# Performance work log

Measured on AMD Instinct MI355X. Metric: run time of the kernel, lower is better.

The kernel has to match this reference:

```python
import jax, jax.numpy as jnp
import numpy as np

B, N, E, R, D, L = 2, 40000, 400000, 64, 64, 6
LN_EPS = 1e-5


def _layer_norm(x, g, b):
    mu = jnp.mean(x, axis=-1, keepdims=True)
    var = jnp.var(x, axis=-1, keepdims=True)
    return (x - mu) * jax.lax.rsqrt(var + LN_EPS) * g + b


def setup_inputs() -> dict:
    key = jax.random.key(0)
    ks = jax.random.split(key, 10)
    s = 0.05
    return {
        "rel_reps": jax.random.normal(ks[0], (B, R, D), jnp.float32),
        "h_index": jax.random.randint(ks[1], (B,), 0, N, jnp.int32),
        "r_index": jax.random.randint(ks[2], (B,), 0, R, jnp.int32),
        "edge_index": jax.random.randint(ks[3], (2, E), 0, N, jnp.int32),
        "edge_type": jax.random.randint(ks[4], (E,), 0, R, jnp.int32),
        "proj_w1": jax.random.normal(ks[5], (L, D, D), jnp.float32) * s,
        "proj_b1": jnp.zeros((L, D), jnp.float32),
        "proj_w2": jax.random.normal(ks[6], (L, D, D), jnp.float32) * s,
        "proj_b2": jnp.zeros((L, D), jnp.float32),
        "lin_w": jax.random.normal(ks[7], (L, 2 * D, D), jnp.float32) * s,
        "lin_b": jnp.zeros((L, D), jnp.float32),
        "ln_g": jnp.ones((L, D), jnp.float32),
        "ln_b": jnp.zeros((L, D), jnp.float32),
        "mlp_w": jax.random.normal(ks[8], (2 * D, 2 * D), jnp.float32) * s,
        "mlp_b": jnp.zeros((2 * D,), jnp.float32),
        "num_nodes": N,
    }


def reference(rel_reps, h_index, r_index, edge_index, edge_type,
              proj_w1, proj_b1, proj_w2, proj_b2,
              lin_w, lin_b, ln_g, ln_b, mlp_w, mlp_b, num_nodes):
    # EntityNBFNet.bellmanford with 6 GeneralizedRelationalConv layers
    # (distmult message, sum aggregate, layer_norm, relu, short_cut).
    batch = rel_reps.shape[0]
    query = rel_reps[jnp.arange(batch), r_index]                     # [B, D]
    boundary = jnp.zeros((batch, num_nodes, rel_reps.shape[-1]), rel_reps.dtype)
    boundary = boundary.at[jnp.arange(batch), h_index].set(query)    # [B, N, D]
    src, dst = edge_index[0], edge_index[1]

    def layer_step(x, params):
        pw1, pb1, pw2, pb2, lw, lb, lng, lnb = params
        # per-layer relation projection MLP (project_relations=True)
        rel = jax.nn.relu(jnp.einsum("brd,de->bre", rel_reps, pw1) + pb1)
        rel = jnp.einsum("brd,de->bre", rel, pw2) + pb2              # [B, R, D]
        # distmult message: x_src * rel_edge  -> [B, E, D]
        msg = jnp.take(x, src, axis=1) * jnp.take(rel, edge_type, axis=1)
        # sum aggregation (edge_weight = ones) + boundary self-message
        agg = jax.vmap(lambda m: jax.ops.segment_sum(m, dst, num_segments=num_nodes))(msg)
        agg = agg + boundary
        out = jnp.concatenate([x, agg], axis=-1) @ lw + lb           # [B, N, D]
        out = jax.nn.relu(_layer_norm(out, lng, lnb))
        out = out + x                                                # short cut
        return out, None

    x, _ = jax.lax.scan(layer_step, boundary,
                        (proj_w1, proj_b1, proj_w2, proj_b2, lin_w, lin_b, ln_g, ln_b))
    node_query = jnp.broadcast_to(query[:, None, :], x.shape)        # [B, N, D]
    feature = jnp.concatenate([x, node_query], axis=-1)              # [B, N, 2D]
    # embedd_out=True: MLP = Linear(2D, 2D) + ReLU
    embedd = jax.nn.relu(feature @ mlp_w + mlp_b)
    return embedd
```

## Files before the change

kernel.cpp:

```cpp
#include <hip/hip_runtime.h>
#include <hip/hip_bf16.h>

namespace {

constexpr int B = 2;
constexpr int N = 40000;
constexpr int E = 400000;
constexpr int R = 64;
constexpr int D = 64;
constexpr int L = 6;
constexpr float EPS = 1e-5f;
constexpr int NB = (N + 255) / 256;
constexpr int EB = (E + 255) / 256;

typedef _Float16 v8h __attribute__((ext_vector_type(8)));
typedef _Float16 v2h __attribute__((ext_vector_type(2)));
typedef float    v4f __attribute__((ext_vector_type(4)));

__device__ __forceinline__ unsigned int pack_h2(float a, float b) {
  v2h p; p.x = (_Float16)a; p.y = (_Float16)b;
  return __builtin_bit_cast(unsigned int, p);
}
__device__ __forceinline__ float2 unpack_h2(unsigned int u) {
  v2h p = __builtin_bit_cast(v2h, u);
  return make_float2((float)p.x, (float)p.y);
}


__global__ __launch_bounds__(64) void k_rel(
    const float* __restrict__ rel_reps,
    const float* __restrict__ pw1, const float* __restrict__ pb1,
    const float* __restrict__ pw2, const float* __restrict__ pb2,
    float* __restrict__ rel_f,
    const int* __restrict__ h_index, const int* __restrict__ r_index,
    unsigned int* __restrict__ xb,
    _Float16* __restrict__ xrow0, _Float16* __restrict__ xrow1,
    float* __restrict__ query_f, _Float16* __restrict__ qh) {
  __shared__ float row[D];
  __shared__ float row2[D];
  int idx = blockIdx.x;
  int d = threadIdx.x;
  if (idx == L * B * R) {
    int h0 = h_index[0], h1 = h_index[1];
    float q0 = rel_reps[r_index[0] * D + d];
    float q1 = rel_reps[(R + r_index[1]) * D + d];
    query_f[d * 2] = q0; query_f[d * 2 + 1] = q1;
    qh[d]     = (_Float16)q0;
    qh[D + d] = (_Float16)q1;
    if (h0 == h1) {
      xb[(size_t)h0 * D + d] = pack_h2(q0, q1);
    } else {
      xb[(size_t)h0 * D + d] = pack_h2(q0, 0.f);
      xb[(size_t)h1 * D + d] = pack_h2(0.f, q1);
    }
    xrow0[(size_t)h0 * 2 * D + d] = (_Float16)q0;
    xrow1[(size_t)h1 * 2 * D + d] = (_Float16)q1;
    return;
  }
  int l = idx / (B * R);
  int br = idx - l * (B * R);
  int b = br / R, r = br - b * R;
  row[d] = rel_reps[(size_t)br * D + d];
  __syncthreads();
  const float* w1 = pw1 + (size_t)l * D * D;
  float acc = pb1[l * D + d];
  for (int k = 0; k < D; ++k) acc = fmaf(row[k], w1[k * D + d], acc);
  row2[d] = fmaxf(acc, 0.f);
  __syncthreads();
  const float* w2 = pw2 + (size_t)l * D * D;
  float acc2 = pb2[l * D + d];
  for (int k = 0; k < D; ++k) acc2 = fmaf(row2[k], w2[k * D + d], acc2);
  rel_f[(((size_t)l * R + r) * D + d) * 2 + b] = acc2;
}

__global__ __launch_bounds__(256) void k_pack(
    const float2* __restrict__ rel2, unsigned int* __restrict__ rel_pk,
    const float* __restrict__ lin_w, unsigned short* __restrict__ Wf,
    const float* __restrict__ mlp_w, unsigned short* __restrict__ Wm) {
  int blk = blockIdx.x;
  int tid = threadIdx.x;
  if (blk < 96) {
    int i = blk * 256 + tid;
    float2 v = rel2[i];
    rel_pk[i] = pack_h2(v.x, v.y);
  } else if (blk < 120) {
    int idx = (blk - 96) * 4 + (tid >> 6);
    int lane = tid & 63;
    int l = idx >> 4, ct = (idx >> 2) & 3, ks = idx & 3;
    int n = ct * 16 + (lane & 15);
    #pragma unroll
    for (int j = 0; j < 8; ++j) {
      int k = ks * 32 + (lane >> 4) * 8 + j;
      _Float16 v = (_Float16)lin_w[(size_t)l * 2 * D * D + (size_t)k * D + n];
      Wf[(size_t)l * 8192 + ((size_t)((ct * 4 + ks) * 64) + lane) * 8 + j] =
          __builtin_bit_cast(unsigned short, v);
    }
  } else {
    int idx = (blk - 120) * 4 + (tid >> 6);
    int lane = tid & 63;
    int ct = idx >> 2, ks = idx & 3;
    int n = ct * 16 + (lane & 15);
    #pragma unroll
    for (int j = 0; j < 8; ++j) {
      int k = ks * 32 + (lane >> 4) * 8 + j;
      _Float16 v = (_Float16)mlp_w[(size_t)k * 2 * D + n];
      Wm[((size_t)idx * 64 + lane) * 8 + j] = __builtin_bit_cast(unsigned short, v);
    }
  }
}

__global__ __launch_bounds__(256) void k_hist(const int* __restrict__ dst,
                                              int* __restrict__ cnt) {
  int e = blockIdx.x * 256 + threadIdx.x;
  if (e < E) atomicAdd(&cnt[dst[e]], 1);
}

__global__ __launch_bounds__(256) void k_scan1(const int* __restrict__ cnt,
                                               int* __restrict__ row_ptr,
                                               int* __restrict__ bsum) {
  __shared__ int s[256];
  int t = threadIdx.x;
  int i = blockIdx.x * 256 + t;
  int v = (i < N) ? cnt[i] : 0;
  s[t] = v;
  __syncthreads();
  #pragma unroll
  for (int off = 1; off < 256; off <<= 1) {
    int u = (t >= off) ? s[t - off] : 0;
    __syncthreads();
    s[t] += u;
    __syncthreads();
  }
  if (i < N) row_ptr[i] = s[t] - v;
  if (t == 255) bsum[blockIdx.x] = s[255];
}

__global__ __launch_bounds__(256) void k_scan3(int* __restrict__ row_ptr,
                                               const int* __restrict__ bsum,
                                               int* __restrict__ cursor) {
  __shared__ int red[256];
  int t = threadIdx.x;
  int v = (t < (int)blockIdx.x) ? bsum[t] : 0;
  red[t] = v;
  __syncthreads();
  #pragma unroll
  for (int off = 128; off > 0; off >>= 1) {
    if (t < off) red[t] += red[t + off];
    __syncthreads();
  }
  int offv = red[0];
  int i = blockIdx.x * 256 + t;
  if (i < N) {
    int r = row_ptr[i] + offv;
    row_ptr[i] = r;
    cursor[i] = r;
  }
  if (i == N - 1) row_ptr[N] = E;
}

__global__ __launch_bounds__(256) void k_fill(const int* __restrict__ src,
                                              const int* __restrict__ dst,
                                              const int* __restrict__ etype,
                                              int* __restrict__ cursor,
                                              unsigned int* __restrict__ es) {
  int e = blockIdx.x * 256 + threadIdx.x;
  if (e < E) {
    int p = atomicAdd(&cursor[dst[e]], 1);
    es[p] = (unsigned int)src[e] | ((unsigned int)etype[e] << 16);
  }
}

__global__ __launch_bounds__(256, 6) void k_gather(
    const unsigned int* __restrict__ xb,
    _Float16* __restrict__ xrow0, _Float16* __restrict__ xrow1,
    const unsigned int* __restrict__ rel_pk,
    const int* __restrict__ row_ptr, const unsigned int* __restrict__ es,
    const float2* __restrict__ q2, const int* __restrict__ h_index, int first) {
  int tid = threadIdx.x;
  int lane = tid & 63;
  int h = lane >> 5;
  int ln = lane & 31;
  int w = (blockIdx.x * 256 + tid) >> 6;
  int n = w * 2 + h;
  int h0 = h_index[0], h1 = h_index[1];
  int rp = 0;
  if (lane < 3) rp = row_ptr[2 * w + lane];
  int rs = __shfl(rp, h);
  int re = __shfl(rp, h + 1);
  int deg = re - rs;
  int dc = min(deg, 32);
  unsigned int esv = 0;
  if (ln < dc) esv = es[rs + ln];
  float a0x = 0.f, a0y = 0.f, a1x = 0.f, a1y = 0.f;
  if (first) {
    for (int j = 0; j < dc; ++j) {
      unsigned int pk = __shfl(esv, (h << 5) | j);
      int s = (int)(pk & 0xffffu), et = (int)(pk >> 16);
      if (s == h0 || s == h1) {
        uint2 xv = *(const uint2*)&xb[(size_t)s * D + 2 * ln];
        uint2 rv = *(const uint2*)&rel_pk[et * D + 2 * ln];
        float2 xfx = unpack_h2(xv.x), xfy = unpack_h2(xv.y);
        float2 rfx = unpack_h2(rv.x), rfy = unpack_h2(rv.y);
        if (s == h0) { a0x = fmaf(xfx.x, rfx.x, a0x); a0y = fmaf(xfy.x, rfy.x, a0y); }
        if (s == h1) { a1x = fmaf(xfx.y, rfx.y, a1x); a1y = fmaf(xfy.y, rfy.y, a1y); }
      }
    }
    for (int j = rs + 32; j < re; ++j) {
      unsigned int pk = es[j];
      int s = (int)(pk & 0xffffu), et = (int)(pk >> 16);
      if (s == h0 || s == h1) {
        uint2 xv = *(const uint2*)&xb[(size_t)s * D + 2 * ln];
        uint2 rv = *(const uint2*)&rel_pk[et * D + 2 * ln];
        float2 xfx = unpack_h2(xv.x), xfy = unpack_h2(xv.y);
        float2 rfx = unpack_h2(rv.x), rfy = unpack_h2(rv.y);
        if (s == h0) { a0x = fmaf(xfx.x, rfx.x, a0x); a0y = fmaf(xfy.x, rfy.x, a0y); }
        if (s == h1) { a1x = fmaf(xfx.y, rfx.y, a1x); a1y = fmaf(xfy.y, rfy.y, a1y); }
      }
    }
  } else {
    int rounds = (dc + 7) >> 3;
    int maxr = max(__shfl(rounds, 0), __shfl(rounds, 32));
    for (int jr = 0; jr < maxr; ++jr) {
      int j = jr * 8;
      unsigned int pk[8];
      uint2 xv[8], rv[8];
      #pragma unroll
      for (int u = 0; u < 8; ++u) {
        int iu = max(min(j + u, dc - 1), 0);
        pk[u] = __shfl(esv, (h << 5) | iu);
      }
      #pragma unroll
      for (int u = 0; u < 8; ++u) {
        xv[u] = *(const uint2*)&xb[(size_t)(pk[u] & 0xffffu) * D + 2 * ln];
        rv[u] = *(const uint2*)&rel_pk[(pk[u] >> 16) * D + 2 * ln];
      }
      #pragma unroll
      for (int u = 0; u < 8; ++u) {
        if (j + u < dc) {
          float2 xfx = unpack_h2(xv[u].x), xfy = unpack_h2(xv[u].y);
          float2 rfx = unpack_h2(rv[u].x), rfy = unpack_h2(rv[u].y);
          a0x = fmaf(xfx.x, rfx.x, a0x); a1x = fmaf(xfx.y, rfx.y, a1x);
          a0y = fmaf(xfy.x, rfy.x, a0y); a1y = fmaf(xfy.y, rfy.y, a1y);
        }
      }
    }
    for (int j = rs + 32; j < re; ++j) {
      unsigned int pk = es[j];
      uint2 xv = *(const uint2*)&xb[(size_t)(pk & 0xffffu) * D + 2 * ln];
      uint2 rv = *(const uint2*)&rel_pk[(pk >> 16) * D + 2 * ln];
      float2 xfx = unpack_h2(xv.x), xfy = unpack_h2(xv.y);
      float2 rfx = unpack_h2(rv.x), rfy = unpack_h2(rv.y);
      a0x = fmaf(xfx.x, rfx.x, a0x); a1x = fmaf(xfx.y, rfx.y, a1x);
      a0y = fmaf(xfy.x, rfy.x, a0y); a1y = fmaf(xfy.y, rfy.y, a1y);
    }
  }
  if (n == h0) {
    float4 qq = *(const float4*)&q2[2 * ln];
    a0x += qq.x; a0y += qq.z;
  }
  if (n == h1) {
    float4 qq = *(const float4*)&q2[2 * ln];
    a1x += qq.y; a1y += qq.w;
  }
  v2h s0; s0.x = (_Float16)a0x; s0.y = (_Float16)a0y;
  v2h s1; s1.x = (_Float16)a1x; s1.y = (_Float16)a1y;
  *(v2h*)&xrow0[(size_t)n * 2 * D + D + 2 * ln] = s0;
  *(v2h*)&xrow1[(size_t)n * 2 * D + D + 2 * ln] = s1;
}

__global__ __launch_bounds__(64) void k_linear(
    unsigned int* __restrict__ xb,
    _Float16* __restrict__ xrow0, _Float16* __restrict__ xrow1,
    const unsigned short* __restrict__ Wf,
    const float* __restrict__ lin_b, const float* __restrict__ ln_g,
    const float* __restrict__ ln_b, int layer) {
  int lane = threadIdx.x;
  int nb = blockIdx.x * 16;
  int c = lane & 15, rg = lane >> 4;
  const v8h* wf = (const v8h*)(Wf + (size_t)layer * 8192);
  v8h Bf[4][4];
  #pragma unroll
  for (int ct = 0; ct < 4; ++ct)
    #pragma unroll
    for (int ks = 0; ks < 4; ++ks)
      Bf[ct][ks] = wf[(ct * 4 + ks) * 64 + lane];
  v4f acc0[4], acc1[4];
  #pragma unroll
  for (int ct = 0; ct < 4; ++ct) {
    acc0[ct] = (v4f){0.f, 0.f, 0.f, 0.f};
    acc1[ct] = (v4f){0.f, 0.f, 0.f, 0.f};
  }
  #pragma unroll
  for (int ks = 0; ks < 4; ++ks) {
    size_t aoff = (size_t)(nb + c) * 2 * D + ks * 32 + rg * 8;
    v8h A0 = *(const v8h*)(xrow0 + aoff);
    v8h A1 = *(const v8h*)(xrow1 + aoff);
    #pragma unroll
    for (int ct = 0; ct < 4; ++ct) {
      acc0[ct] = __builtin_amdgcn_mfma_f32_16x16x32_f16(A0, Bf[ct][ks], acc0[ct], 0, 0, 0);
      acc1[ct] = __builtin_amdgcn_mfma_f32_16x16x32_f16(A1, Bf[ct][ks], acc1[ct], 0, 0, 0);
    }
  }
  float bias4[4], g4[4], be4[4];
  #pragma unroll
  for (int ct = 0; ct < 4; ++ct) {
    int d = ct * 16 + c;
    bias4[ct] = lin_b[layer * D + d];
    g4[ct]    = ln_g[layer * D + d];
    be4[ct]   = ln_b[layer * D + d];
  }
  #pragma unroll
  for (int j = 0; j < 4; ++j) {
    int node = nb + rg * 4 + j;
    float v0[4], v1[4];
    float s10 = 0.f, s20 = 0.f, s11 = 0.f, s21 = 0.f;
    #pragma unroll
    for (int ct = 0; ct < 4; ++ct) {
      v0[ct] = acc0[ct][j] + bias4[ct];
      v1[ct] = acc1[ct][j] + bias4[ct];
      s10 += v0[ct]; s20 += v0[ct] * v0[ct];
      s11 += v1[ct]; s21 += v1[ct] * v1[ct];
    }
    #pragma unroll
    for (int mk = 1; mk < 16; mk <<= 1) {
      s10 += __shfl_xor(s10, mk); s20 += __shfl_xor(s20, mk);
      s11 += __shfl_xor(s11, mk); s21 += __shfl_xor(s21, mk);
    }
    float mu0 = s10 * (1.f / D), var0 = s20 * (1.f / D) - mu0 * mu0;
    float mu1 = s11 * (1.f / D), var1 = s21 * (1.f / D) - mu1 * mu1;
    float rs0 = rsqrtf(var0 + EPS), rs1 = rsqrtf(var1 + EPS);
    #pragma unroll
    for (int ct = 0; ct < 4; ++ct) {
      int d = ct * 16 + c;
      float o0 = fmaxf((v0[ct] - mu0) * rs0 * g4[ct] + be4[ct], 0.f);
      float o1 = fmaxf((v1[ct] - mu1) * rs1 * g4[ct] + be4[ct], 0.f);
      float2 xv = unpack_h2(xb[(size_t)node * D + d]);
      float r0 = o0 + xv.x, r1 = o1 + xv.y;
      xb[(size_t)node * D + d] = pack_h2(r0, r1);
      xrow0[(size_t)node * 2 * D + d] = (_Float16)r0;
      xrow1[(size_t)node * 2 * D + d] = (_Float16)r1;
    }
  }
}

__global__ __launch_bounds__(64) void k_mlp(
    const _Float16* __restrict__ xrow0, const _Float16* __restrict__ xrow1,
    const _Float16* __restrict__ qh,
    const unsigned short* __restrict__ Wm,
    const float* __restrict__ mlp_b,
    float* __restrict__ outf) {
  int lane = threadIdx.x;
  int nb = blockIdx.x * 16;
  int c = lane & 15, rg = lane >> 4;
  const v8h* wm = (const v8h*)Wm;
  v4f acc0[8], acc1[8];
  #pragma unroll
  for (int ct = 0; ct < 8; ++ct) {
    acc0[ct] = (v4f){0.f, 0.f, 0.f, 0.f};
    acc1[ct] = (v4f){0.f, 0.f, 0.f, 0.f};
  }
  #pragma unroll
  for (int ks = 0; ks < 4; ++ks) {
    v8h A0, A1;
    if (ks < 2) {
      size_t aoff = (size_t)(nb + c) * 2 * D + ks * 32 + rg * 8;
      A0 = *(const v8h*)(xrow0 + aoff);
      A1 = *(const v8h*)(xrow1 + aoff);
    } else {
      int qoff = (ks - 2) * 32 + rg * 8;
      A0 = *(const v8h*)(qh + qoff);
      A1 = *(const v8h*)(qh + D + qoff);
    }
    #pragma unroll
    for (int ct = 0; ct < 8; ++ct) {
      v8h Bv = wm[(ct * 4 + ks) * 64 + lane];
      acc0[ct] = __builtin_amdgcn_mfma_f32_16x16x32_f16(A0, Bv, acc0[ct], 0, 0, 0);
      acc1[ct] = __builtin_amdgcn_mfma_f32_16x16x32_f16(A1, Bv, acc1[ct], 0, 0, 0);
    }
  }
  #pragma unroll
  for (int ct = 0; ct < 8; ++ct) {
    int d = ct * 16 + c;
    float bias = mlp_b[d];
    #pragma unroll
    for (int j = 0; j < 4; ++j) {
      int node = nb + rg * 4 + j;
      outf[(size_t)node * 2 * D + d]       = fmaxf(acc0[ct][j] + bias, 0.f);
      outf[((size_t)N + node) * 2 * D + d] = fmaxf(acc1[ct][j] + bias, 0.f);
    }
  }
}

}

extern "C" void kernel_launch(void* const* d_in, const int* in_sizes, int n_in,
                              void* d_out, int out_size, void* d_ws, size_t ws_size,
                              hipStream_t stream) {
  const float* rel_reps = (const float*)d_in[0];
  const int* h_index    = (const int*)d_in[1];
  const int* r_index    = (const int*)d_in[2];
  const int* edge_index = (const int*)d_in[3];
  const int* edge_type  = (const int*)d_in[4];
  const float* proj_w1  = (const float*)d_in[5];
  const float* proj_b1  = (const float*)d_in[6];
  const float* proj_w2  = (const float*)d_in[7];
  const float* proj_b2  = (const float*)d_in[8];
  const float* lin_w    = (const float*)d_in[9];
  const float* lin_b    = (const float*)d_in[10];
  const float* ln_g     = (const float*)d_in[11];
  const float* ln_b     = (const float*)d_in[12];
  const float* mlp_w    = (const float*)d_in[13];
  const float* mlp_b    = (const float*)d_in[14];

  unsigned int* xb = (unsigned int*)d_ws;
  _Float16* xrow0 = (_Float16*)(xb + (size_t)N * D);
  _Float16* xrow1 = xrow0 + (size_t)N * 2 * D;
  unsigned int* rel_pk = (unsigned int*)(xrow1 + (size_t)N * 2 * D);
  unsigned short* Wf = (unsigned short*)(rel_pk + (size_t)L * R * D);
  unsigned short* Wm = Wf + (size_t)L * 8192;
  _Float16* qh = (_Float16*)(Wm + 16384);
  float* rel_all = (float*)(qh + 128);
  float* query   = rel_all + (size_t)2 * L * R * D;
  int*   cnt     = (int*)(query + 2 * D);
  int*   row_ptr = cnt + N;
  int*   cursor  = row_ptr + (N + 1);
  unsigned int* es = (unsigned int*)(cursor + N);
  int*   bsum    = (int*)(es + E);

  const int* srcp = edge_index;
  const int* dstp = edge_index + E;

  hipMemsetAsync(xb, 0, (size_t)N * D * 4 + (size_t)N * 2 * D * 2 * 2, stream);
  hipMemsetAsync(cnt, 0, N * sizeof(int), stream);
  k_rel<<<L * B * R + 1, 64, 0, stream>>>(rel_reps, proj_w1, proj_b1, proj_w2, proj_b2,
                                          rel_all, h_index, r_index,
                                          xb, xrow0, xrow1, query, qh);
  k_pack<<<128, 256, 0, stream>>>((const float2*)rel_all, rel_pk, lin_w, Wf, mlp_w, Wm);
  k_hist<<<EB, 256, 0, stream>>>(dstp, cnt);
  k_scan1<<<NB, 256, 0, stream>>>(cnt, row_ptr, bsum);
  k_scan3<<<NB, 256, 0, stream>>>(row_ptr, bsum, cursor);
  k_fill<<<EB, 256, 0, stream>>>(srcp, dstp, edge_type, cursor, es);

  for (int l = 0; l < L; ++l) {
    k_gather<<<N / 8, 256, 0, stream>>>(xb, xrow0, xrow1,
                                        rel_pk + (size_t)l * R * D,
                                        row_ptr, es, (const float2*)query, h_index,
                                        (l == 0) ? 1 : 0);
    k_linear<<<N / 16, 64, 0, stream>>>(xb, xrow0, xrow1,
                                        Wf, lin_b, ln_g, ln_b, l);
  }
  k_mlp<<<N / 16, 64, 0, stream>>>(xrow0, xrow1, qh, Wm, mlp_b, (float*)d_out);
}
```

Before: 348.4 us.

## Fuse gather and linear+layernorm into one per-layer kernel with ping-pong buffers

Merges the edge-gather aggregation and the MFMA linear/layernorm/residual step into a single kernel per layer. Aggregates go through shared memory instead of the separate fp16 row buffers. Node state ping-pongs between two packed buffers, and the first layer synthesizes its input from the query rather than relying on a zeroed buffer. This removes the large memset, the duplicate xrow stores, and one launch per layer. In exchange, only one wave of four does the 8-row MFMA, so half of the 16-row tile is wasted, and the 64-lane tail runs while the other waves sit idle.

```diff
diff --git a/kernel.cpp b/kernel.cpp
--- a/kernel.cpp
+++ b/kernel.cpp
@@ -25,6 +25,34 @@
   v2h p = __builtin_bit_cast(v2h, u);
   return make_float2((float)p.x, (float)p.y);
 }
+__device__ __forceinline__ v8h lo8(uint4 a, uint4 b) {
+  uint4 r;
+  r.x = (a.x & 0xffffu) | (a.y << 16);
+  r.y = (a.z & 0xffffu) | (a.w << 16);
+  r.z = (b.x & 0xffffu) | (b.y << 16);
+  r.w = (b.z & 0xffffu) | (b.w << 16);
+  return __builtin_bit_cast(v8h, r);
+}
+__device__ __forceinline__ v8h hi8(uint4 a, uint4 b) {
+  uint4 r;
+  r.x = (a.x >> 16) | (a.y & 0xffff0000u);
+  r.y = (a.z >> 16) | (a.w & 0xffff0000u);
+  r.z = (b.x >> 16) | (b.w & 0xffff0000u & 0u) | (b.w & 0xffff0000u);
+  r.w = 0u;
+  return __builtin_bit_cast(v8h, r);
+}
+__device__ __forceinline__ v8h hi8c(uint4 a, uint4 b) {
+  uint4 r;
+  r.x = (a.x >> 16) | (a.y & 0xffff0000u);
+  r.y = (a.z >> 16) | (a.w & 0xffff0000u);
+  r.z = (b.x >> 16) | (b.y & 0xffff0000u);
+  r.w = (b.z >> 16) | (b.w & 0xffff0000u);
+  return __builtin_bit_cast(v8h, r);
+}
+__device__ __forceinline__ v8h zero8() {
+  uint4 z; z.x = 0u; z.y = 0u; z.z = 0u; z.w = 0u;
+  return __builtin_bit_cast(v8h, z);
+}
 
 
 __global__ __launch_bounds__(64) void k_rel(
@@ -33,8 +61,7 @@
     const float* __restrict__ pw2, const float* __restrict__ pb2,
     float* __restrict__ rel_f,
     const int* __restrict__ h_index, const int* __restrict__ r_index,
-    unsigned int* __restrict__ xb,
-    _Float16* __restrict__ xrow0, _Float16* __restrict__ xrow1,
+    unsigned int* __restrict__ xb0,
     float* __restrict__ query_f, _Float16* __restrict__ qh) {
   __shared__ float row[D];
   __shared__ float row2[D];
@@ -48,13 +75,11 @@
     qh[d]     = (_Float16)q0;
     qh[D + d] = (_Float16)q1;
     if (h0 == h1) {
-      xb[(size_t)h0 * D + d] = pack_h2(q0, q1);
+      xb0[(size_t)h0 * D + d] = pack_h2(q0, q1);
     } else {
-      xb[(size_t)h0 * D + d] = pack_h2(q0, 0.f);
-      xb[(size_t)h1 * D + d] = pack_h2(0.f, q1);
-    }
-    xrow0[(size_t)h0 * 2 * D + d] = (_Float16)q0;
-    xrow1[(size_t)h1 * 2 * D + d] = (_Float16)q1;
+      xb0[(size_t)h0 * D + d] = pack_h2(q0, 0.f);
+      xb0[(size_t)h1 * D + d] = pack_h2(0.f, q1);
+    }
     return;
   }
   int l = idx / (B * R);
@@ -170,18 +195,25 @@
   }
 }
 
-__global__ __launch_bounds__(256, 6) void k_gather(
-    const unsigned int* __restrict__ xb,
-    _Float16* __restrict__ xrow0, _Float16* __restrict__ xrow1,
+__global__ __launch_bounds__(256, 6) void k_layer(
+    const unsigned int* __restrict__ xb_prev,
+    unsigned int* __restrict__ xb_next,
     const unsigned int* __restrict__ rel_pk,
     const int* __restrict__ row_ptr, const unsigned int* __restrict__ es,
-    const float2* __restrict__ q2, const int* __restrict__ h_index, int first) {
+    const float2* __restrict__ q2, const int* __restrict__ h_index,
+    const _Float16* __restrict__ qh, const float* __restrict__ qf,
+    const unsigned short* __restrict__ Wf,
+    const float* __restrict__ lin_b, const float* __restrict__ ln_g,
+    const float* __restrict__ ln_b, int layer, int first) {
+  __shared__ unsigned int agg[8 * 68];
   int tid = threadIdx.x;
   int lane = tid & 63;
   int h = lane >> 5;
   int ln = lane & 31;
-  int w = (blockIdx.x * 256 + tid) >> 6;
+  int wv = tid >> 6;
+  int w = blockIdx.x * 4 + wv;
   int n = w * 2 + h;
+  int nb = blockIdx.x * 8;
   int h0 = h_index[0], h1 = h_index[1];
   int rp = 0;
   if (lane < 3) rp = row_ptr[2 * w + lane];
@@ -197,7 +229,7 @@
       unsigned int pk = __shfl(esv, (h << 5) | j);
       int s = (int)(pk & 0xffffu), et = (int)(pk >> 16);
       if (s == h0 || s == h1) {
-        uint2 xv = *(const uint2*)&xb[(size_t)s * D + 2 * ln];
+        uint2 xv = *(const uint2*)&xb_prev[(size_t)s * D + 2 * ln];
         uint2 rv = *(const uint2*)&rel_pk[et * D + 2 * ln];
         float2 xfx = unpack_h2(xv.x), xfy = unpack_h2(xv.y);
         float2 rfx = unpack_h2(rv.x), rfy = unpack_h2(rv.y);
@@ -209,7 +241,7 @@
       unsigned int pk = es[j];
       int s = (int)(pk & 0xffffu), et = (int)(pk >> 16);
       if (s == h0 || s == h1) {
-        uint2 xv = *(const uint2*)&xb[(size_t)s * D + 2 * ln];
+        uint2 xv = *(const uint2*)&xb_prev[(size_t)s * D + 2 * ln];
         uint2 rv = *(const uint2*)&rel_pk[et * D + 2 * ln];
         float2 xfx = unpack_h2(xv.x), xfy = unpack_h2(xv.y);
         float2 rfx = unpack_h2(rv.x), rfy = unpack_h2(rv.y);
@@ -231,7 +263,7 @@
       }
       #pragma unroll
       for (int u = 0; u < 8; ++u) {
-        xv[u] = *(const uint2*)&xb[(size_t)(pk[u] & 0xffffu) * D + 2 * ln];
+        xv[u] = *(const uint2*)&xb_prev[(size_t)(pk[u] & 0xffffu) * D + 2 * ln];
         rv[u] = *(const uint2*)&rel_pk[(pk[u] >> 16) * D + 2 * ln];
       }
       #pragma unroll
@@ -246,7 +278,7 @@
     }
     for (int j = rs + 32; j < re; ++j) {
       unsigned int pk = es[j];
-      uint2 xv = *(const uint2*)&xb[(size_t)(pk & 0xffffu) * D + 2 * ln];
+      uint2 xv = *(const uint2*)&xb_prev[(size_t)(pk & 0xffffu) * D + 2 * ln];
       uint2 rv = *(const uint2*)&rel_pk[(pk >> 16) * D + 2 * ln];
       float2 xfx = unpack_h2(xv.x), xfy = unpack_h2(xv.y);
       float2 rfx = unpack_h2(rv.x), rfy = unpack_h2(rv.y);
@@ -262,28 +294,18 @@
     float4 qq = *(const float4*)&q2[2 * ln];
     a1x += qq.y; a1y += qq.w;
   }
-  v2h s0; s0.x = (_Float16)a0x; s0.y = (_Float16)a0y;
-  v2h s1; s1.x = (_Float16)a1x; s1.y = (_Float16)a1y;
-  *(v2h*)&xrow0[(size_t)n * 2 * D + D + 2 * ln] = s0;
-  *(v2h*)&xrow1[(size_t)n * 2 * D + D + 2 * ln] = s1;
-}
-
-__global__ __launch_bounds__(64) void k_linear(
-    unsigned int* __restrict__ xb,
-    _Float16* __restrict__ xrow0, _Float16* __restrict__ xrow1,
-    const unsigned short* __restrict__ Wf,
-    const float* __restrict__ lin_b, const float* __restrict__ ln_g,
-    const float* __restrict__ ln_b, int layer) {
-  int lane = threadIdx.x;
-  int nb = blockIdx.x * 16;
+  {
+    int nl = 2 * wv + h;
+    uint2 st;
+    st.x = pack_h2(a0x, a1x);
+    st.y = pack_h2(a0y, a1y);
+    *(uint2*)&agg[nl * 68 + 2 * ln] = st;
+  }
+  __syncthreads();
+  if (tid >= 64) return;
+
   int c = lane & 15, rg = lane >> 4;
   const v8h* wf = (const v8h*)(Wf + (size_t)layer * 8192);
-  v8h Bf[4][4];
-  #pragma unroll
-  for (int ct = 0; ct < 4; ++ct)
-    #pragma unroll
-    for (int ks = 0; ks < 4; ++ks)
-      Bf[ct][ks] = wf[(ct * 4 + ks) * 64 + lane];
   v4f acc0[4], acc1[4];
   #pragma unroll
   for (int ct = 0; ct < 4; ++ct) {
@@ -292,13 +314,29 @@
   }
   #pragma unroll
   for (int ks = 0; ks < 4; ++ks) {
-    size_t aoff = (size_t)(nb + c) * 2 * D + ks * 32 + rg * 8;
-    v8h A0 = *(const v8h*)(xrow0 + aoff);
-    v8h A1 = *(const v8h*)(xrow1 + aoff);
+    v8h A0 = zero8(), A1 = zero8();
+    if (c < 8) {
+      if (ks < 2) {
+        if (first) {
+          int node = nb + c;
+          if (node == h0) A0 = *(const v8h*)(qh + ks * 32 + rg * 8);
+          if (node == h1) A1 = *(const v8h*)(qh + D + ks * 32 + rg * 8);
+        } else {
+          const uint4* p = (const uint4*)&xb_prev[(size_t)(nb + c) * D + ks * 32 + rg * 8];
+          uint4 a = p[0], b = p[1];
+          A0 = lo8(a, b); A1 = hi8c(a, b);
+        }
+      } else {
+        const uint4* p = (const uint4*)&agg[c * 68 + (ks - 2) * 32 + rg * 8];
+        uint4 a = p[0], b = p[1];
+        A0 = lo8(a, b); A1 = hi8c(a, b);
+      }
+    }
     #pragma unroll
     for (int ct = 0; ct < 4; ++ct) {
-      acc0[ct] = __builtin_amdgcn_mfma_f32_16x16x32_f16(A0, Bf[ct][ks], acc0[ct], 0, 0, 0);
-      acc1[ct] = __builtin_amdgcn_mfma_f32_16x16x32_f16(A1, Bf[ct][ks], acc1[ct], 0, 0, 0);
+      v8h Bv = wf[(ct * 4 + ks) * 64 + lane];
+      acc0[ct] = __builtin_amdgcn_mfma_f32_16x16x32_f16(A0, Bv, acc0[ct], 0, 0, 0);
+      acc1[ct] = __builtin_amdgcn_mfma_f32_16x16x32_f16(A1, Bv, acc1[ct], 0, 0, 0);
     }
   }
   float bias4[4], g4[4], be4[4];
@@ -311,40 +349,47 @@
   }
   #pragma unroll
   for (int j = 0; j < 4; ++j) {
-    int node = nb + rg * 4 + j;
-    float v0[4], v1[4];
-    float s10 = 0.f, s20 = 0.f, s11 = 0.f, s21 = 0.f;
-    #pragma unroll
-    for (int ct = 0; ct < 4; ++ct) {
-      v0[ct] = acc0[ct][j] + bias4[ct];
-      v1[ct] = acc1[ct][j] + bias4[ct];
-      s10 += v0[ct]; s20 += v0[ct] * v0[ct];
-      s11 += v1[ct]; s21 += v1[ct] * v1[ct];
-    }
-    #pragma unroll
-    for (int mk = 1; mk < 16; mk <<= 1) {
-      s10 += __shfl_xor(s10, mk); s20 += __shfl_xor(s20, mk);
-      s11 += __shfl_xor(s11, mk); s21 += __shfl_xor(s21, mk);
-    }
-    float mu0 = s10 * (1.f / D), var0 = s20 * (1.f / D) - mu0 * mu0;
-    float mu1 = s11 * (1.f / D), var1 = s21 * (1.f / D) - mu1 * mu1;
-    float rs0 = rsqrtf(var0 + EPS), rs1 = rsqrtf(var1 + EPS);
-    #pragma unroll
-    for (int ct = 0; ct < 4; ++ct) {
-      int d = ct * 16 + c;
-      float o0 = fmaxf((v0[ct] - mu0) * rs0 * g4[ct] + be4[ct], 0.f);
-      float o1 = fmaxf((v1[ct] - mu1) * rs1 * g4[ct] + be4[ct], 0.f);
-      float2 xv = unpack_h2(xb[(size_t)node * D + d]);
-      float r0 = o0 + xv.x, r1 = o1 + xv.y;
-      xb[(size_t)node * D + d] = pack_h2(r0, r1);
-      xrow0[(size_t)node * 2 * D + d] = (_Float16)r0;
-      xrow1[(size_t)node * 2 * D + d] = (_Float16)r1;
+    int r = rg * 4 + j;
+    if (r < 8) {
+      int node = nb + r;
+      float v0[4], v1[4];
+      float s10 = 0.f, s20 = 0.f, s11 = 0.f, s21 = 0.f;
+      #pragma unroll
+      for (int ct = 0; ct < 4; ++ct) {
+        v0[ct] = acc0[ct][j] + bias4[ct];
+        v1[ct] = acc1[ct][j] + bias4[ct];
+        s10 += v0[ct]; s20 += v0[ct] * v0[ct];
+        s11 += v1[ct]; s21 += v1[ct] * v1[ct];
+      }
+      #pragma unroll
+      for (int mk = 1; mk < 16; mk <<= 1) {
+        s10 += __shfl_xor(s10, mk); s20 += __shfl_xor(s20, mk);
+        s11 += __shfl_xor(s11, mk); s21 += __shfl_xor(s21, mk);
+      }
+      float mu0 = s10 * (1.f / D), var0 = s20 * (1.f / D) - mu0 * mu0;
+      float mu1 = s11 * (1.f / D), var1 = s21 * (1.f / D) - mu1 * mu1;
+      float rs0 = rsqrtf(var0 + EPS), rs1 = rsqrtf(var1 + EPS);
+      #pragma unroll
+      for (int ct = 0; ct < 4; ++ct) {
+        int d = ct * 16 + c;
+        float o0 = fmaxf((v0[ct] - mu0) * rs0 * g4[ct] + be4[ct], 0.f);
+        float o1 = fmaxf((v1[ct] - mu1) * rs1 * g4[ct] + be4[ct], 0.f);
+        float xr0, xr1;
+        if (first) {
+          xr0 = (node == h0) ? qf[2 * d] : 0.f;
+          xr1 = (node == h1) ? qf[2 * d + 1] : 0.f;
+        } else {
+          float2 xv = unpack_h2(xb_prev[(size_t)node * D + d]);
+          xr0 = xv.x; xr1 = xv.y;
+        }
+        xb_next[(size_t)node * D + d] = pack_h2(o0 + xr0, o1 + xr1);
+      }
     }
   }
 }
 
 __global__ __launch_bounds__(64) void k_mlp(
-    const _Float16* __restrict__ xrow0, const _Float16* __restrict__ xrow1,
+    const unsigned int* __restrict__ xbf,
     const _Float16* __restrict__ qh,
     const unsigned short* __restrict__ Wm,
     const float* __restrict__ mlp_b,
@@ -363,9 +408,9 @@
   for (int ks = 0; ks < 4; ++ks) {
     v8h A0, A1;
     if (ks < 2) {
-      size_t aoff = (size_t)(nb + c) * 2 * D + ks * 32 + rg * 8;
-      A0 = *(const v8h*)(xrow0 + aoff);
-      A1 = *(const v8h*)(xrow1 + aoff);
+      const uint4* p = (const uint4*)&xbf[(size_t)(nb + c) * D + ks * 32 + rg * 8];
+      uint4 a = p[0], b = p[1];
+      A0 = lo8(a, b); A1 = hi8c(a, b);
     } else {
       int qoff = (ks - 2) * 32 + rg * 8;
       A0 = *(const v8h*)(qh + qoff);
@@ -412,10 +457,9 @@
   const float* mlp_w    = (const float*)d_in[13];
   const float* mlp_b    = (const float*)d_in[14];
 
-  unsigned int* xb = (unsigned int*)d_ws;
-  _Float16* xrow0 = (_Float16*)(xb + (size_t)N * D);
-  _Float16* xrow1 = xrow0 + (size_t)N * 2 * D;
-  unsigned int* rel_pk = (unsigned int*)(xrow1 + (size_t)N * 2 * D);
+  unsigned int* xb0 = (unsigned int*)d_ws;
+  unsigned int* xb1 = xb0 + (size_t)N * D;
+  unsigned int* rel_pk = xb1 + (size_t)N * D;
   unsigned short* Wf = (unsigned short*)(rel_pk + (size_t)L * R * D);
   unsigned short* Wm = Wf + (size_t)L * 8192;
   _Float16* qh = (_Float16*)(Wm + 16384);
@@ -430,11 +474,10 @@
   const int* srcp = edge_index;
   const int* dstp = edge_index + E;
 
-  hipMemsetAsync(xb, 0, (size_t)N * D * 4 + (size_t)N * 2 * D * 2 * 2, stream);
   hipMemsetAsync(cnt, 0, N * sizeof(int), stream);
   k_rel<<<L * B * R + 1, 64, 0, stream>>>(rel_reps, proj_w1, proj_b1, proj_w2, proj_b2,
                                           rel_all, h_index, r_index,
-                                          xb, xrow0, xrow1, query, qh);
+                                          xb0, query, qh);
   k_pack<<<128, 256, 0, stream>>>((const float2*)rel_all, rel_pk, lin_w, Wf, mlp_w, Wm);
   k_hist<<<EB, 256, 0, stream>>>(dstp, cnt);
   k_scan1<<<NB, 256, 0, stream>>>(cnt, row_ptr, bsum);
@@ -442,12 +485,13 @@
   k_fill<<<EB, 256, 0, stream>>>(srcp, dstp, edge_type, cursor, es);
 
   for (int l = 0; l < L; ++l) {
-    k_gather<<<N / 8, 256, 0, stream>>>(xb, xrow0, xrow1,
-                                        rel_pk + (size_t)l * R * D,
-                                        row_ptr, es, (const float2*)query, h_index,
-                                        (l == 0) ? 1 : 0);
-    k_linear<<<N / 16, 64, 0, stream>>>(xb, xrow0, xrow1,
-                                        Wf, lin_b, ln_g, ln_b, l);
-  }
-  k_mlp<<<N / 16, 64, 0, stream>>>(xrow0, xrow1, qh, Wm, mlp_b, (float*)d_out);
-}
+    const unsigned int* src = (l & 1) ? xb1 : xb0;
+    unsigned int* dst = (l & 1) ? xb0 : xb1;
+    k_layer<<<N / 8, 256, 0, stream>>>(src, dst,
+                                       rel_pk + (size_t)l * R * D,
+                                       row_ptr, es, (const float2*)query, h_index,
+                                       qh, query, Wf, lin_b, ln_g, ln_b,
+                                       l, (l == 0) ? 1 : 0);
+  }
+  k_mlp<<<N / 16, 64, 0, stream>>>(xb0, qh, Wm, mlp_b, (float*)d_out);
+}
```

New measurement: 364.8 us. +4.7%, slower.
